# Optimization experiments

Measured on AMD Instinct MI355X. Metric: run time of the kernel, lower is better.

The kernel has to match this reference:

```python
import jax, jax.numpy as jnp
import numpy as np

PST_THD = 0.05
NMS_THD = 0.5
TOP_K = 1000  # max candidates kept before greedy NMS (fixed for jit)
IMG = 1024
NUM_CLASSES = 80


def _make_anchors(H, W):
    # Standard RetinaNet anchors: P3-P7, 3 ratios x 3 scales = 9 per location.
    levels = [3, 4, 5, 6, 7]
    ratios = np.array([0.5, 1.0, 2.0])
    scales = np.array([2 ** 0, 2 ** (1.0 / 3.0), 2 ** (2.0 / 3.0)])
    all_a = []
    for l in levels:
        stride = 2 ** l
        size = 2 ** (l + 2)
        base = []
        for r in ratios:
            for s in scales:
                area = (size * s) ** 2
                w = np.sqrt(area / r)
                h = w * r
                base.append([-w / 2, -h / 2, w / 2, h / 2])
        base = np.asarray(base)  # (9,4)
        fh, fw = H // stride, W // stride
        sx = (np.arange(fw) + 0.5) * stride
        sy = (np.arange(fh) + 0.5) * stride
        sxx, syy = np.meshgrid(sx, sy)
        shifts = np.stack([sxx.ravel(), syy.ravel(), sxx.ravel(), syy.ravel()], 1)
        all_a.append((shifts[:, None, :] + base[None, :, :]).reshape(-1, 4))
    return np.concatenate(all_a, 0).astype(np.float32)  # (A,4)


def setup_inputs() -> dict:
    key = jax.random.key(0)
    k1, k2 = jax.random.split(key)
    anchors = jnp.asarray(_make_anchors(IMG, IMG))  # (A,4)
    A = anchors.shape[0]
    classification = jax.random.uniform(k1, (1, A, NUM_CLASSES), dtype=jnp.float32)
    regression = jax.random.normal(k2, (1, A, 4), dtype=jnp.float32) * 0.5
    return {
        "classification": classification,
        "regression": regression,
        "anchors": anchors,
        "height": IMG,
        "width": IMG,
    }


def _postprocess(classification, regression, anchors, height, width):
    cls = classification[0]   # (A,C)
    reg = regression[0]       # (A,4)
    # --- BBoxTransform (std = [0.1,0.1,0.2,0.2]) ---
    wa = anchors[:, 2] - anchors[:, 0]
    ha = anchors[:, 3] - anchors[:, 1]
    cxa = anchors[:, 0] + 0.5 * wa
    cya = anchors[:, 1] + 0.5 * ha
    pcx = cxa + reg[:, 0] * 0.1 * wa
    pcy = cya + reg[:, 1] * 0.1 * ha
    pw = jnp.exp(reg[:, 2] * 0.2) * wa
    ph = jnp.exp(reg[:, 3] * 0.2) * ha
    # --- ClipBoxes ---
    x1 = jnp.clip(pcx - 0.5 * pw, 0.0, None)
    y1 = jnp.clip(pcy - 0.5 * ph, 0.0, None)
    x2 = jnp.minimum(pcx + 0.5 * pw, jnp.float32(width))
    y2 = jnp.minimum(pcy + 0.5 * ph, jnp.float32(height))
    boxes = jnp.stack([x1, y1, x2, y2], axis=1)  # (A,4)
    # --- score threshold + top-K candidate selection ---
    scores = jnp.max(cls, axis=1)
    class_id = jnp.argmax(cls, axis=1).astype(jnp.int32)
    masked = jnp.where(scores > PST_THD, scores, -1.0)
    top_s, idx = jax.lax.top_k(masked, TOP_K)  # sorted descending
    b = boxes[idx]                             # (K,4)
    c = class_id[idx]
    valid = top_s > PST_THD
    # --- greedy NMS over K candidates (classic py_cpu_nms, +1 areas) ---
    area = (b[:, 2] - b[:, 0] + 1.0) * (b[:, 3] - b[:, 1] + 1.0)
    xx1 = jnp.maximum(b[:, None, 0], b[None, :, 0])
    yy1 = jnp.maximum(b[:, None, 1], b[None, :, 1])
    xx2 = jnp.minimum(b[:, None, 2], b[None, :, 2])
    yy2 = jnp.minimum(b[:, None, 3], b[None, :, 3])
    inter = jnp.clip(xx2 - xx1 + 1.0, 0.0) * jnp.clip(yy2 - yy1 + 1.0, 0.0)
    iou = inter / (area[:, None] + area[None, :] - inter)  # (K,K)
    later = jnp.arange(TOP_K)

    def body(i, keep):
        supp = (iou[i] > NMS_THD) & (later > i) & keep[i]
        return keep & (~supp)

    keep = jax.lax.fori_loop(0, TOP_K, body, valid)
    nms_scores = jnp.where(keep, top_s, 0.0)
    nms_classes = jnp.where(keep, c, -1)
    nms_boxes = jnp.where(keep[:, None], b, 0.0)
    return nms_scores, nms_classes, nms_boxes


def reference(classification, regression, anchors, height, width):
    # Fixed-size padded equivalent of the original variable-length NMS output.
    return _postprocess(classification, regression, anchors, height, width)
```

## Files before the change

kernel.cpp:

```cpp
#include <hip/hip_runtime.h>
#include <stdint.h>

#define K_TOP 1000
#define PST 0.05f
#define THR 256
#define NTAIL 64
#define ROWS 128
#define PADW 81

#define C_DONE0 0
#define C_BAR   4
#define C_CNTA  6
#define C_CNTE  7
#define C_PREFIX 8
#define C_CUM    9

typedef unsigned long long ull;

__device__ __forceinline__ unsigned mapU(float f) {
  unsigned b = __float_as_uint(f);
  return (b & 0x80000000u) ? ~b : (b | 0x80000000u);
}
__device__ __forceinline__ float unmapU(unsigned u) {
  unsigned b = (u & 0x80000000u) ? (u ^ 0x80000000u) : ~u;
  return __uint_as_float(b);
}
__device__ __forceinline__ float scalar_dim(const int* p) {
  int v = *p;
  if (v > 0 && v < (1 << 20)) return (float)v;
  return __int_as_float(v);
}

__device__ __forceinline__ unsigned aldU(const unsigned* p) {
  return __hip_atomic_load(p, __ATOMIC_RELAXED, __HIP_MEMORY_SCOPE_AGENT);
}
__device__ __forceinline__ void astU(unsigned* p, unsigned v) {
  __hip_atomic_store(p, v, __ATOMIC_RELAXED, __HIP_MEMORY_SCOPE_AGENT);
}
__device__ __forceinline__ ull aldL(const ull* p) {
  return __hip_atomic_load(p, __ATOMIC_RELAXED, __HIP_MEMORY_SCOPE_AGENT);
}
__device__ __forceinline__ void astL(ull* p, ull v) {
  __hip_atomic_store(p, v, __ATOMIC_RELAXED, __HIP_MEMORY_SCOPE_AGENT);
}

__device__ __forceinline__ void gsync(unsigned* bar, unsigned target) {
  __syncthreads();
  if (threadIdx.x == 0) {
    __hip_atomic_fetch_add(bar, 1u, __ATOMIC_RELAXED, __HIP_MEMORY_SCOPE_AGENT);
    while (__hip_atomic_load(bar, __ATOMIC_RELAXED, __HIP_MEMORY_SCOPE_AGENT) < target)
      __builtin_amdgcn_s_sleep(1);
  }
  __syncthreads();
}

template <int NB>
__device__ void selectN(const unsigned* __restrict__ histL, int shift,
                        unsigned* __restrict__ ctrl) {
  constexpr int PB = NB / 64;
  int t = threadIdx.x;
  unsigned cumIn = ctrl[C_CUM];
  unsigned need = (unsigned)K_TOP - cumIn;
  unsigned h[PB];
  unsigned v = 0;
  #pragma unroll
  for (int b = 0; b < PB; ++b) { h[b] = histL[PB * t + b]; v += h[b]; }
  #pragma unroll
  for (int d = 1; d < 64; d <<= 1) {
    unsigned q = __shfl_down(v, d);
    if (t + d < 64) v += q;
  }
  unsigned sn = __shfl_down(v, 1);
  if (t == 63) sn = 0;
  if (v >= need && sn < need) {
    unsigned c = sn;
    int bsel = PB * t;
    for (int b = PB - 1; b >= 0; --b) {
      if (c + h[b] >= need) { bsel = PB * t + b; break; }
      c += h[b];
    }
    ctrl[C_PREFIX] = ctrl[C_PREFIX] | (((unsigned)bsel) << shift);
    ctrl[C_CUM] = cumIn + c;
  }
}

template <int NB>
__device__ void selectL(const unsigned* __restrict__ histL, int shift,
                        unsigned* sPref, unsigned* sCum) {
  constexpr int PB = NB / 64;
  int t = threadIdx.x;
  unsigned cumIn = *sCum;
  unsigned need = (unsigned)K_TOP - cumIn;
  unsigned h[PB];
  unsigned v = 0;
  #pragma unroll
  for (int b = 0; b < PB; ++b) { h[b] = aldU(&histL[PB * t + b]); v += h[b]; }
  #pragma unroll
  for (int d = 1; d < 64; d <<= 1) {
    unsigned q = __shfl_down(v, d);
    if (t + d < 64) v += q;
  }
  unsigned sn = __shfl_down(v, 1);
  if (t == 63) sn = 0;
  if (v >= need && sn < need) {
    unsigned c = sn;
    int bsel = PB * t;
    for (int b = PB - 1; b >= 0; --b) {
      if (c + h[b] >= need) { bsel = PB * t + b; break; }
      c += h[b];
    }
    *sPref = *sPref | (((unsigned)bsel) << shift);
    *sCum = cumIn + c;
  }
}

__device__ __forceinline__ void decode_box(int a, const float4* anc4,
                                           const float4* reg4, float W, float H,
                                           float4* boxes) {
  float4 an = anc4[a];
  float4 rg = reg4[a];
  float wa = an.z - an.x, ha = an.w - an.y;
  float cxa = an.x + 0.5f * wa, cya = an.y + 0.5f * ha;
  float pcx = cxa + rg.x * 0.1f * wa;
  float pcy = cya + rg.y * 0.1f * ha;
  float pw = expf(rg.z * 0.2f) * wa;
  float ph = expf(rg.w * 0.2f) * ha;
  float x1 = fmaxf(pcx - 0.5f * pw, 0.f);
  float y1 = fmaxf(pcy - 0.5f * ph, 0.f);
  float x2 = fminf(pcx + 0.5f * pw, W);
  float y2 = fminf(pcy + 0.5f * ph, H);
  boxes[a] = make_float4(x1, y1, x2, y2);
}

__global__ void __launch_bounds__(1024) k_init(unsigned* hist, unsigned* ctrl,
                                               ull* keyBuf, float* candS,
                                               int* candC, float4* candB) {
  int t = threadIdx.x;
  for (int e = t; e < 5120; e += 1024) hist[e] = 0u;
  if (t < 64) ctrl[t] = 0u;
  for (int e = t; e < 4096; e += 1024) keyBuf[e] = 0ull;
  candS[t] = -1.0f;
  candC[t] = -1;
  candB[t] = make_float4(0.f, 0.f, 0.f, 0.f);
}

__global__ void __launch_bounds__(THR) k_decode_staged(
    const float* __restrict__ cls, const float* __restrict__ reg,
    const float* __restrict__ anc, const int* __restrict__ hp,
    const int* __restrict__ wp, int A,
    float4* __restrict__ boxes, unsigned* __restrict__ su,
    int* __restrict__ ci, unsigned* hist0, unsigned* ctrl, int nb) {
  __shared__ float s[ROWS * PADW];
  __shared__ unsigned lh[2048];
  int t = threadIdx.x;
  int r0 = blockIdx.x * ROWS;
  for (int b = t; b < 2048; b += THR) lh[b] = 0u;

  const float4* g4 = (const float4*)cls;
  #pragma unroll
  for (int i = 0; i < 10; ++i) {
    int f = t + THR * i;
    int row = f / 20, c4 = f % 20;
    if (r0 + row < A) {
      float4 v = g4[(size_t)r0 * 20 + f];
      int base = row * PADW + c4 * 4;
      s[base + 0] = v.x; s[base + 1] = v.y; s[base + 2] = v.z; s[base + 3] = v.w;
    }
  }
  __syncthreads();

  if (t < ROWS) {
    int a = r0 + t;
    if (a < A) {
      const float* rowp = s + t * PADW;
      float m = rowp[0]; int mi = 0;
      #pragma unroll
      for (int j = 1; j < 80; ++j) {
        float v = rowp[j];
        if (v > m) { m = v; mi = j; }
      }
      float W = scalar_dim(wp), H = scalar_dim(hp);
      decode_box(a, (const float4*)anc, (const float4*)reg, W, H, boxes);
      ci[a] = mi;
      float msk = (m > PST) ? m : -1.0f;
      unsigned u = mapU(msk);
      su[a] = u;
      atomicAdd(&lh[u >> 21], 1u);
    }
  }
  __syncthreads();
  for (int b = t; b < 2048; b += THR)
    if (lh[b]) atomicAdd(&hist0[b], lh[b]);
  __shared__ int last;
  __syncthreads();
  if (t == 0) {
    unsigned old = __hip_atomic_fetch_add(&ctrl[C_DONE0], 1u,
                                          __ATOMIC_ACQ_REL, __HIP_MEMORY_SCOPE_AGENT);
    last = (old == (unsigned)(nb - 1));
  }
  __syncthreads();
  if (last && t < 64) selectN<2048>(hist0, 21, ctrl);
}

__global__ void __launch_bounds__(THR) k_decode_generic(
    const float* __restrict__ cls, const float* __restrict__ reg,
    const float* __restrict__ anc, const int* __restrict__ hp,
    const int* __restrict__ wp, int A, int C,
    float4* __restrict__ boxes, unsigned* __restrict__ su,
    int* __restrict__ ci, unsigned* hist0, unsigned* ctrl, int nb) {
  __shared__ unsigned lh[2048];
  int t = threadIdx.x;
  for (int b = t; b < 2048; b += THR) lh[b] = 0u;
  __syncthreads();
  int a = blockIdx.x * THR + t;
  if (a < A) {
    const float* row = cls + (size_t)a * C;
    float m = -3.4e38f; int mi = 0;
    for (int j = 0; j < C; ++j) { float v = row[j]; if (v > m) { m = v; mi = j; } }
    float W = scalar_dim(wp), H = scalar_dim(hp);
    decode_box(a, (const float4*)anc, (const float4*)reg, W, H, boxes);
    ci[a] = mi;
    float msk = (m > PST) ? m : -1.0f;
    unsigned u = mapU(msk);
    su[a] = u;
    atomicAdd(&lh[u >> 21], 1u);
  }
  __syncthreads();
  for (int b = t; b < 2048; b += THR)
    if (lh[b]) atomicAdd(&hist0[b], lh[b]);
  __shared__ int last;
  __syncthreads();
  if (t == 0) {
    unsigned old = __hip_atomic_fetch_add(&ctrl[C_DONE0], 1u,
                                          __ATOMIC_ACQ_REL, __HIP_MEMORY_SCOPE_AGENT);
    last = (old == (unsigned)(nb - 1));
  }
  __syncthreads();
  if (last && t < 64) selectN<2048>(hist0, 21, ctrl);
}

__global__ void __launch_bounds__(THR) k_tail(
    const unsigned* __restrict__ su, int A,
    const float4* __restrict__ boxes, const int* __restrict__ ci,
    ull* __restrict__ keyBuf, float* __restrict__ candS,
    int* __restrict__ candC, float4* __restrict__ candB,
    ull* __restrict__ maskBuf, unsigned* hist, unsigned* ctrl,
    float* __restrict__ out) {
  __shared__ ull shmem[2048];
  __shared__ ull keepW[16];
  __shared__ unsigned lh[2048];
  __shared__ unsigned sPref, sCum;
  int t = threadIdx.x;
  int g0 = blockIdx.x * THR + t;

  if (t == 0) { sPref = ctrl[C_PREFIX]; sCum = ctrl[C_CUM]; }

  for (int b = t; b < 2048; b += THR) lh[b] = 0u;
  __syncthreads();
  unsigned pref = sPref;
  for (int a = g0; a < A; a += NTAIL * THR) {
    unsigned u = su[a];
    if ((u & 0xFFE00000u) == pref) atomicAdd(&lh[(u >> 10) & 2047u], 1u);
  }
  __syncthreads();
  for (int b = t; b < 2048; b += THR)
    if (lh[b]) atomicAdd(&hist[2048 + b], lh[b]);
  gsync(&ctrl[C_BAR], NTAIL);
  if (t < 64) selectL<2048>(hist + 2048, 10, &sPref, &sCum);
  __syncthreads();

  for (int b = t; b < 1024; b += THR) lh[b] = 0u;
  __syncthreads();
  pref = sPref;
  for (int a = g0; a < A; a += NTAIL * THR) {
    unsigned u = su[a];
    if ((u & 0xFFFFFC00u) == pref) atomicAdd(&lh[u & 1023u], 1u);
  }
  __syncthreads();
  for (int b = t; b < 1024; b += THR)
    if (lh[b]) atomicAdd(&hist[4096 + b], lh[b]);
  gsync(&ctrl[C_BAR], 2 * NTAIL);
  if (t < 64) selectL<1024>(hist + 4096, 0, &sPref, &sCum);
  __syncthreads();
  unsigned uT = sPref;

  for (int a = g0; a < A; a += NTAIL * THR) {
    unsigned u = su[a];
    if (u > uT) {
      unsigned p = atomicAdd(&ctrl[C_CNTA], 1u);
      if (p < 1000u) astL(&keyBuf[p], (((ull)u) << 32) | (unsigned)(~a));
    } else if (u == uT) {
      unsigned p = atomicAdd(&ctrl[C_CNTE], 1u);
      if (p < 3072u) astL(&keyBuf[1024 + p], (((ull)u) << 32) | (unsigned)(~a));
    }
  }
  gsync(&ctrl[C_BAR], 3 * NTAIL);

  unsigned nTop = aldU(&ctrl[C_CNTA]);
  unsigned nTie = aldU(&ctrl[C_CNTE]); if (nTie > 3072u) nTie = 3072u;
  for (int e = t; e < 1024; e += THR) shmem[e] = aldL(&keyBuf[e]);
  __syncthreads();
  int wid = t >> 6, lane = t & 63;
  int gw = blockIdx.x * 4 + wid;
  #pragma unroll
  for (int s2 = 0; s2 < 4; ++s2) {
    int sidx = gw * 4 + s2;
    ull k0 = shmem[sidx];
    if (k0 != 0ull) {
      unsigned cnt = 0;
      for (int e = lane; e < 1024; e += 64) cnt += (shmem[e] > k0) ? 1u : 0u;
      #pragma unroll
      for (int d = 32; d; d >>= 1) cnt += __shfl_down(cnt, d);
      if (lane == 0 && cnt < (unsigned)K_TOP) {
        unsigned idx = ~(unsigned)k0;
        float4 bb = boxes[idx];
        astU((unsigned*)&candS[cnt], __float_as_uint(unmapU((unsigned)(k0 >> 32))));
        astU((unsigned*)&candC[cnt], (unsigned)ci[idx]);
        ull* bp = (ull*)&candB[cnt];
        astL(bp, ((ull)__float_as_uint(bb.y) << 32) | __float_as_uint(bb.x));
        astL(bp + 1, ((ull)__float_as_uint(bb.w) << 32) | __float_as_uint(bb.z));
      }
    }
  }
  for (int tix = gw; tix < (int)nTie; tix += NTAIL * 4) {
    ull k0 = aldL(&keyBuf[1024 + tix]);
    unsigned cnt = 0;
    for (int e = lane; e < (int)nTie; e += 64)
      cnt += (aldL(&keyBuf[1024 + e]) > k0) ? 1u : 0u;
    #pragma unroll
    for (int d = 32; d; d >>= 1) cnt += __shfl_down(cnt, d);
    if (lane == 0) {
      unsigned rank = nTop + cnt;
      if (rank < (unsigned)K_TOP) {
        unsigned idx = ~(unsigned)k0;
        float4 bb = boxes[idx];
        astU((unsigned*)&candS[rank], __float_as_uint(unmapU((unsigned)(k0 >> 32))));
        astU((unsigned*)&candC[rank], (unsigned)ci[idx]);
        ull* bp = (ull*)&candB[rank];
        astL(bp, ((ull)__float_as_uint(bb.y) << 32) | __float_as_uint(bb.x));
        astL(bp + 1, ((ull)__float_as_uint(bb.w) << 32) | __float_as_uint(bb.z));
      }
    }
  }
  gsync(&ctrl[C_BAR], 4 * NTAIL);

  float4* sCand = (float4*)shmem;
  for (int e = t; e < 1024; e += THR) {
    const ull* bp = (const ull*)&candB[e];
    ull lo = aldL(bp), hi = aldL(bp + 1);
    sCand[e] = make_float4(__uint_as_float((unsigned)lo),
                           __uint_as_float((unsigned)(lo >> 32)),
                           __uint_as_float((unsigned)hi),
                           __uint_as_float((unsigned)(hi >> 32)));
  }
  __syncthreads();
  {
    int g4 = blockIdx.x * THR + t;
    int i = g4 & 1023, w = g4 >> 10;
    float4 bi = sCand[i];
    float areai = (bi.z - bi.x + 1.f) * (bi.w - bi.y + 1.f);
    ull bits = 0ull;
    if (i < K_TOP) {
      int j0 = w << 6;
      #pragma unroll 4
      for (int b = 0; b < 64; ++b) {
        int j = j0 + b;
        if (j > i && j < K_TOP) {
          float4 bj = sCand[j];
          float xx1 = fmaxf(bi.x, bj.x);
          float yy1 = fmaxf(bi.y, bj.y);
          float xx2 = fminf(bi.z, bj.z);
          float yy2 = fminf(bi.w, bj.w);
          float iw = fmaxf(xx2 - xx1 + 1.f, 0.f);
          float ih = fmaxf(yy2 - yy1 + 1.f, 0.f);
          float inter = iw * ih;
          float areaj = (bj.z - bj.x + 1.f) * (bj.w - bj.y + 1.f);
          float iou = inter / (areai + areaj - inter);
          if (iou > 0.5f) bits |= (1ull << b);
        }
      }
    }
    astL(&maskBuf[i * 16 + w], bits);
  }
  gsync(&ctrl[C_BAR], 5 * NTAIL);

  if (blockIdx.x != 0) return;
  ull (*buf)[1024] = (ull(*)[1024])shmem;
  __syncthreads();
  for (int e = t; e < 1024; e += THR) buf[0][e] = aldL(&maskBuf[e]);
  __syncthreads();

  unsigned long long remv = 0ull;
  int l = t & 63;
  if (t < 64 && l < 16) {
    ull vb = 0ull;
    for (int b = 0; b < 64; ++b) {
      float s = __uint_as_float(aldU((const unsigned*)&candS[(l << 6) + b]));
      if (s > PST) vb |= (1ull << b);
    }
    remv = ~vb;
  }
  for (int w = 0; w < 16; ++w) {
    if (w + 1 < 16 && t >= 64) {
      for (int e = t - 64; e < 1024; e += THR - 64)
        buf[(w + 1) & 1][e] = aldL(&maskBuf[(w + 1) * 1024 + e]);
    }
    if (t < 64) {
      ull cw = __shfl(remv, w);
      const ull* rows = buf[w & 1];
      #pragma unroll
      for (int b = 0; b < 64; ++b) {
        ull mrow = rows[b * 16 + (l & 15)];
        ull mvw  = rows[b * 16 + w];
        ull sel = ((cw >> b) & 1ull) - 1ull;
        remv |= (mrow & sel);
        cw   |= (mvw & sel);
      }
    }
    __syncthreads();
  }
  if (t < 64 && l < 16) keepW[l] = ~remv;
  __syncthreads();

  for (int q = t; q < K_TOP; q += THR) {
    bool kp = (keepW[q >> 6] >> (q & 63)) & 1ull;
    float sc = __uint_as_float(aldU((const unsigned*)&candS[q]));
    int cc = (int)aldU((const unsigned*)&candC[q]);
    const ull* bp = (const ull*)&candB[q];
    ull lo = aldL(bp), hi = aldL(bp + 1);
    out[q] = kp ? sc : 0.f;
    out[K_TOP + q] = kp ? (float)cc : -1.f;
    float4 ob = kp ? make_float4(__uint_as_float((unsigned)lo),
                                 __uint_as_float((unsigned)(lo >> 32)),
                                 __uint_as_float((unsigned)hi),
                                 __uint_as_float((unsigned)(hi >> 32)))
                   : make_float4(0.f, 0.f, 0.f, 0.f);
    *(float4*)(out + 2 * K_TOP + 4 * q) = ob;
  }
}

extern "C" void kernel_launch(void* const* d_in, const int* in_sizes, int n_in,
                              void* d_out, int out_size, void* d_ws, size_t ws_size,
                              hipStream_t stream) {
  const float* cls = (const float*)d_in[0];
  const float* reg = (const float*)d_in[1];
  const float* anc = (const float*)d_in[2];
  const int* hp = (const int*)d_in[3];
  const int* wp = (const int*)d_in[4];
  int A = in_sizes[2] / 4;
  int C = in_sizes[0] / A;

  char* ws = (char*)d_ws;
  size_t off = 0;
  auto alloc = [&](size_t bytes) -> void* {
    void* p = ws + off;
    off = (off + bytes + 255) & ~(size_t)255;
    return p;
  };
  float4* boxes = (float4*)alloc((size_t)A * 16);
  unsigned* su = (unsigned*)alloc((size_t)A * 4);
  int* ci = (int*)alloc((size_t)A * 4);
  ull* keyBuf = (ull*)alloc(4096 * 8);
  float* candS = (float*)alloc(1024 * 4);
  int* candC = (int*)alloc(1024 * 4);
  float4* candB = (float4*)alloc(1024 * 16);
  ull* maskBuf = (ull*)alloc(16384 * 8);
  unsigned* hist = (unsigned*)alloc(5120 * 4);
  unsigned* ctrl = (unsigned*)alloc(256 * 4);
  (void)ws_size; (void)n_in; (void)out_size;

  hipLaunchKernelGGL(k_init, dim3(1), dim3(1024), 0, stream,
                     hist, ctrl, keyBuf, candS, candC, candB);
  if (C == 80) {
    int nb = (A + ROWS - 1) / ROWS;
    hipLaunchKernelGGL(k_decode_staged, dim3(nb), dim3(THR), 0, stream,
                       cls, reg, anc, hp, wp, A,
                       boxes, su, ci, hist, ctrl, nb);
  } else {
    int nb = (A + THR - 1) / THR;
    hipLaunchKernelGGL(k_decode_generic, dim3(nb), dim3(THR), 0, stream,
                       cls, reg, anc, hp, wp, A, C,
                       boxes, su, ci, hist, ctrl, nb);
  }
  hipLaunchKernelGGL(k_tail, dim3(NTAIL), dim3(THR), 0, stream,
                     su, A, boxes, ci, keyBuf, candS, candC, candB,
                     maskBuf, hist, ctrl, (float*)d_out);
}
```

Baseline: 228.4 us.

## Replace staged decode with per-thread float4 argmax and split tail kernel

The shared-memory staged decode for C==80 is dropped. A single decode kernel now has one thread per anchor that reads its class row with float4 loads. The monolithic tail kernel is split into a selection kernel and an NMS kernel, so a kernel boundary replaces one grid-wide barrier. Global histogram flushes are rotated per block to spread atomic contention, and the valid-bit mask is built with a wavefront ballot instead of a serial loop. The per-thread row reads are uncoalesced (320-byte stride across lanes) and may cost more than the shared-memory staging did, and the extra launch adds overhead.

```diff
diff --git a/kernel.cpp b/kernel.cpp
--- a/kernel.cpp
+++ b/kernel.cpp
@@ -5,11 +5,10 @@
 #define PST 0.05f
 #define THR 256
 #define NTAIL 64
-#define ROWS 128
-#define PADW 81
 
 #define C_DONE0 0
 #define C_BAR   4
+#define C_BAR2  5
 #define C_CNTA  6
 #define C_CNTE  7
 #define C_PREFIX 8
@@ -114,24 +113,6 @@
   }
 }
 
-__device__ __forceinline__ void decode_box(int a, const float4* anc4,
-                                           const float4* reg4, float W, float H,
-                                           float4* boxes) {
-  float4 an = anc4[a];
-  float4 rg = reg4[a];
-  float wa = an.z - an.x, ha = an.w - an.y;
-  float cxa = an.x + 0.5f * wa, cya = an.y + 0.5f * ha;
-  float pcx = cxa + rg.x * 0.1f * wa;
-  float pcy = cya + rg.y * 0.1f * ha;
-  float pw = expf(rg.z * 0.2f) * wa;
-  float ph = expf(rg.w * 0.2f) * ha;
-  float x1 = fmaxf(pcx - 0.5f * pw, 0.f);
-  float y1 = fmaxf(pcy - 0.5f * ph, 0.f);
-  float x2 = fminf(pcx + 0.5f * pw, W);
-  float y2 = fminf(pcy + 0.5f * ph, H);
-  boxes[a] = make_float4(x1, y1, x2, y2);
-}
-
 __global__ void __launch_bounds__(1024) k_init(unsigned* hist, unsigned* ctrl,
                                                ull* keyBuf, float* candS,
                                                int* candC, float4* candB) {
@@ -144,65 +125,7 @@
   candB[t] = make_float4(0.f, 0.f, 0.f, 0.f);
 }
 
-__global__ void __launch_bounds__(THR) k_decode_staged(
-    const float* __restrict__ cls, const float* __restrict__ reg,
-    const float* __restrict__ anc, const int* __restrict__ hp,
-    const int* __restrict__ wp, int A,
-    float4* __restrict__ boxes, unsigned* __restrict__ su,
-    int* __restrict__ ci, unsigned* hist0, unsigned* ctrl, int nb) {
-  __shared__ float s[ROWS * PADW];
-  __shared__ unsigned lh[2048];
-  int t = threadIdx.x;
-  int r0 = blockIdx.x * ROWS;
-  for (int b = t; b < 2048; b += THR) lh[b] = 0u;
-
-  const float4* g4 = (const float4*)cls;
-  #pragma unroll
-  for (int i = 0; i < 10; ++i) {
-    int f = t + THR * i;
-    int row = f / 20, c4 = f % 20;
-    if (r0 + row < A) {
-      float4 v = g4[(size_t)r0 * 20 + f];
-      int base = row * PADW + c4 * 4;
-      s[base + 0] = v.x; s[base + 1] = v.y; s[base + 2] = v.z; s[base + 3] = v.w;
-    }
-  }
-  __syncthreads();
-
-  if (t < ROWS) {
-    int a = r0 + t;
-    if (a < A) {
-      const float* rowp = s + t * PADW;
-      float m = rowp[0]; int mi = 0;
-      #pragma unroll
-      for (int j = 1; j < 80; ++j) {
-        float v = rowp[j];
-        if (v > m) { m = v; mi = j; }
-      }
-      float W = scalar_dim(wp), H = scalar_dim(hp);
-      decode_box(a, (const float4*)anc, (const float4*)reg, W, H, boxes);
-      ci[a] = mi;
-      float msk = (m > PST) ? m : -1.0f;
-      unsigned u = mapU(msk);
-      su[a] = u;
-      atomicAdd(&lh[u >> 21], 1u);
-    }
-  }
-  __syncthreads();
-  for (int b = t; b < 2048; b += THR)
-    if (lh[b]) atomicAdd(&hist0[b], lh[b]);
-  __shared__ int last;
-  __syncthreads();
-  if (t == 0) {
-    unsigned old = __hip_atomic_fetch_add(&ctrl[C_DONE0], 1u,
-                                          __ATOMIC_ACQ_REL, __HIP_MEMORY_SCOPE_AGENT);
-    last = (old == (unsigned)(nb - 1));
-  }
-  __syncthreads();
-  if (last && t < 64) selectN<2048>(hist0, 21, ctrl);
-}
-
-__global__ void __launch_bounds__(THR) k_decode_generic(
+__global__ void __launch_bounds__(THR) k_decode(
     const float* __restrict__ cls, const float* __restrict__ reg,
     const float* __restrict__ anc, const int* __restrict__ hp,
     const int* __restrict__ wp, int A, int C,
@@ -216,9 +139,30 @@
   if (a < A) {
     const float* row = cls + (size_t)a * C;
     float m = -3.4e38f; int mi = 0;
-    for (int j = 0; j < C; ++j) { float v = row[j]; if (v > m) { m = v; mi = j; } }
+    int j = 0;
+    for (; j + 4 <= C; j += 4) {
+      float4 v = *(const float4*)(row + j);
+      if (v.x > m) { m = v.x; mi = j; }
+      if (v.y > m) { m = v.y; mi = j + 1; }
+      if (v.z > m) { m = v.z; mi = j + 2; }
+      if (v.w > m) { m = v.w; mi = j + 3; }
+    }
+    for (; j < C; ++j) { float v = row[j]; if (v > m) { m = v; mi = j; } }
+
+    float4 an = ((const float4*)anc)[a];
+    float4 rg = ((const float4*)reg)[a];
+    float wa = an.z - an.x, ha = an.w - an.y;
+    float cxa = an.x + 0.5f * wa, cya = an.y + 0.5f * ha;
+    float pcx = cxa + rg.x * 0.1f * wa;
+    float pcy = cya + rg.y * 0.1f * ha;
+    float pw = expf(rg.z * 0.2f) * wa;
+    float ph = expf(rg.w * 0.2f) * ha;
     float W = scalar_dim(wp), H = scalar_dim(hp);
-    decode_box(a, (const float4*)anc, (const float4*)reg, W, H, boxes);
+    float x1 = fmaxf(pcx - 0.5f * pw, 0.f);
+    float y1 = fmaxf(pcy - 0.5f * ph, 0.f);
+    float x2 = fminf(pcx + 0.5f * pw, W);
+    float y2 = fminf(pcy + 0.5f * ph, H);
+    boxes[a] = make_float4(x1, y1, x2, y2);
     ci[a] = mi;
     float msk = (m > PST) ? m : -1.0f;
     unsigned u = mapU(msk);
@@ -239,20 +183,13 @@
   if (last && t < 64) selectN<2048>(hist0, 21, ctrl);
 }
 
-__global__ void __launch_bounds__(THR) k_tail(
-    const unsigned* __restrict__ su, int A,
-    const float4* __restrict__ boxes, const int* __restrict__ ci,
-    ull* __restrict__ keyBuf, float* __restrict__ candS,
-    int* __restrict__ candC, float4* __restrict__ candB,
-    ull* __restrict__ maskBuf, unsigned* hist, unsigned* ctrl,
-    float* __restrict__ out) {
-  __shared__ ull shmem[2048];
-  __shared__ ull keepW[16];
+__global__ void __launch_bounds__(THR) k_sel(
+    const unsigned* __restrict__ su, int A, ull* __restrict__ keyBuf,
+    unsigned* hist, unsigned* ctrl) {
   __shared__ unsigned lh[2048];
   __shared__ unsigned sPref, sCum;
   int t = threadIdx.x;
   int g0 = blockIdx.x * THR + t;
-
   if (t == 0) { sPref = ctrl[C_PREFIX]; sCum = ctrl[C_CUM]; }
 
   for (int b = t; b < 2048; b += THR) lh[b] = 0u;
@@ -263,8 +200,13 @@
     if ((u & 0xFFE00000u) == pref) atomicAdd(&lh[(u >> 10) & 2047u], 1u);
   }
   __syncthreads();
-  for (int b = t; b < 2048; b += THR)
-    if (lh[b]) atomicAdd(&hist[2048 + b], lh[b]);
+  {
+    int rot = (blockIdx.x * 331) & 2047;
+    for (int k = 0; k < 2048; k += THR) {
+      int b = (rot + k + t) & 2047;
+      if (lh[b]) atomicAdd(&hist[2048 + b], lh[b]);
+    }
+  }
   gsync(&ctrl[C_BAR], NTAIL);
   if (t < 64) selectL<2048>(hist + 2048, 10, &sPref, &sCum);
   __syncthreads();
@@ -277,8 +219,13 @@
     if ((u & 0xFFFFFC00u) == pref) atomicAdd(&lh[u & 1023u], 1u);
   }
   __syncthreads();
-  for (int b = t; b < 1024; b += THR)
-    if (lh[b]) atomicAdd(&hist[4096 + b], lh[b]);
+  {
+    int rot = (blockIdx.x * 331) & 1023;
+    for (int k = 0; k < 1024; k += THR) {
+      int b = (rot + k + t) & 1023;
+      if (lh[b]) atomicAdd(&hist[4096 + b], lh[b]);
+    }
+  }
   gsync(&ctrl[C_BAR], 2 * NTAIL);
   if (t < 64) selectL<1024>(hist + 4096, 0, &sPref, &sCum);
   __syncthreads();
@@ -294,7 +241,17 @@
       if (p < 3072u) astL(&keyBuf[1024 + p], (((ull)u) << 32) | (unsigned)(~a));
     }
   }
-  gsync(&ctrl[C_BAR], 3 * NTAIL);
+}
+
+__global__ void __launch_bounds__(THR) k_nmsall(
+    const ull* __restrict__ keyBuf, const float4* __restrict__ boxes,
+    const int* __restrict__ ci, int A, float* __restrict__ candS,
+    int* __restrict__ candC, float4* __restrict__ candB,
+    ull* __restrict__ maskBuf, unsigned* ctrl, float* __restrict__ out) {
+  __shared__ ull shmem[2048];
+  __shared__ ull keepW[16];
+  __shared__ ull vbW[16];
+  int t = threadIdx.x;
 
   unsigned nTop = aldU(&ctrl[C_CNTA]);
   unsigned nTie = aldU(&ctrl[C_CNTE]); if (nTie > 3072u) nTie = 3072u;
@@ -342,7 +299,7 @@
       }
     }
   }
-  gsync(&ctrl[C_BAR], 4 * NTAIL);
+  gsync(&ctrl[C_BAR2], NTAIL);
 
   float4* sCand = (float4*)shmem;
   for (int e = t; e < 1024; e += THR) {
@@ -382,24 +339,22 @@
     }
     astL(&maskBuf[i * 16 + w], bits);
   }
-  gsync(&ctrl[C_BAR], 5 * NTAIL);
+  gsync(&ctrl[C_BAR2], 2 * NTAIL);
 
   if (blockIdx.x != 0) return;
   ull (*buf)[1024] = (ull(*)[1024])shmem;
   __syncthreads();
+  for (int q = t; q < 1024; q += THR) {
+    float s = __uint_as_float(aldU((const unsigned*)&candS[q]));
+    ull mball = __ballot(s > PST);
+    if ((q & 63) == 0) vbW[q >> 6] = mball;
+  }
   for (int e = t; e < 1024; e += THR) buf[0][e] = aldL(&maskBuf[e]);
   __syncthreads();
 
-  unsigned long long remv = 0ull;
+  ull remv = 0ull;
   int l = t & 63;
-  if (t < 64 && l < 16) {
-    ull vb = 0ull;
-    for (int b = 0; b < 64; ++b) {
-      float s = __uint_as_float(aldU((const unsigned*)&candS[(l << 6) + b]));
-      if (s > PST) vb |= (1ull << b);
-    }
-    remv = ~vb;
-  }
+  if (t < 64 && l < 16) remv = ~vbW[l];
   for (int w = 0; w < 16; ++w) {
     if (w + 1 < 16 && t >= 64) {
       for (int e = t - 64; e < 1024; e += THR - 64)
@@ -469,20 +424,16 @@
   unsigned* ctrl = (unsigned*)alloc(256 * 4);
   (void)ws_size; (void)n_in; (void)out_size;
 
+  int nb = (A + THR - 1) / THR;
+
   hipLaunchKernelGGL(k_init, dim3(1), dim3(1024), 0, stream,
                      hist, ctrl, keyBuf, candS, candC, candB);
-  if (C == 80) {
-    int nb = (A + ROWS - 1) / ROWS;
-    hipLaunchKernelGGL(k_decode_staged, dim3(nb), dim3(THR), 0, stream,
-                       cls, reg, anc, hp, wp, A,
-                       boxes, su, ci, hist, ctrl, nb);
-  } else {
-    int nb = (A + THR - 1) / THR;
-    hipLaunchKernelGGL(k_decode_generic, dim3(nb), dim3(THR), 0, stream,
-                       cls, reg, anc, hp, wp, A, C,
-                       boxes, su, ci, hist, ctrl, nb);
-  }
-  hipLaunchKernelGGL(k_tail, dim3(NTAIL), dim3(THR), 0, stream,
-                     su, A, boxes, ci, keyBuf, candS, candC, candB,
-                     maskBuf, hist, ctrl, (float*)d_out);
-}
+  hipLaunchKernelGGL(k_decode, dim3(nb), dim3(THR), 0, stream,
+                     cls, reg, anc, hp, wp, A, C,
+                     boxes, su, ci, hist, ctrl, nb);
+  hipLaunchKernelGGL(k_sel, dim3(NTAIL), dim3(THR), 0, stream,
+                     su, A, keyBuf, hist, ctrl);
+  hipLaunchKernelGGL(k_nmsall, dim3(NTAIL), dim3(THR), 0, stream,
+                     keyBuf, boxes, ci, A, candS, candC, candB,
+                     maskBuf, ctrl, (float*)d_out);
+}
```

Result: faster. 223.5 us (-2.1%).
